# Optimization experiments

Measured on AMD Instinct MI355X. Metric: run time of the kernel, lower is better.

The kernel has to match this reference:

```python
import jax, jax.numpy as jnp
import numpy as np

N_NODES = 100000
N_EDGES = 1600000


def setup_inputs() -> dict:
    key = jax.random.key(0)
    ks = jax.random.split(key, 6)
    x = jax.random.normal(ks[0], (N_NODES, 128), dtype=jnp.float32)
    src = jax.random.randint(ks[1], (N_EDGES,), 0, N_NODES, dtype=jnp.int32)
    dst = jax.random.randint(ks[2], (N_EDGES,), 0, N_NODES, dtype=jnp.int32)
    # Glorot-ish scaled weights
    W1 = jax.random.normal(ks[3], (128, 64), dtype=jnp.float32) / np.sqrt(128.0)
    b1 = jnp.zeros((64,), dtype=jnp.float32)
    W2 = jax.random.normal(ks[4], (64, 64), dtype=jnp.float32) / np.sqrt(64.0)
    b2 = jnp.zeros((64,), dtype=jnp.float32)
    return {"x": x, "src": src, "dst": dst, "W1": W1, "b1": b1, "W2": W2, "b2": b2}


def _gcn_forward(x, src_f, dst_f, norm_src, norm_dst, W1, b1, W2, b2):
    n = x.shape[0]

    def conv(h, W, b):
        # weight-first (in_feats >= out_feats in DGL GraphConv): h W is cheap, aggregate small dim
        h = h @ W                                  # [N, d_out]
        h = h * norm_src[:, None]                  # D_out^{-1/2} on source side
        msg = h[src_f]                             # gather per edge [E+N, d_out]
        agg = jax.ops.segment_sum(msg, dst_f, num_segments=n)  # scatter-add to dst
        return agg * norm_dst[:, None] + b         # D_in^{-1/2} + bias

    h = jax.nn.relu(conv(x, W1, b1))
    return conv(h, W2, b2)


def reference(x, src, dst, W1, b1, W2, b2):
    n = x.shape[0]
    loop = jnp.arange(n, dtype=src.dtype)
    src_f = jnp.concatenate([src, loop])  # dgl.add_self_loop
    dst_f = jnp.concatenate([dst, loop])
    ones = jnp.ones(src_f.shape[0], dtype=x.dtype)
    out_deg = jax.ops.segment_sum(ones, src_f, num_segments=n)
    in_deg = jax.ops.segment_sum(ones, dst_f, num_segments=n)
    norm_src = jax.lax.rsqrt(out_deg)  # deg >= 1 due to self loops
    norm_dst = jax.lax.rsqrt(in_deg)
    return _gcn_forward(x, src_f, dst_f, norm_src, norm_dst, W1, b1, W2, b2)
```

## Files before the change

kernel.cpp:

```cpp
#include <hip/hip_runtime.h>
#include <hip/hip_fp16.h>

#define D 64
#define SLICE 25000
#define NBUCK 512
#define EPB 4096

typedef __attribute__((ext_vector_type(8))) short short8;
typedef __attribute__((ext_vector_type(4))) float floatx4;

__global__ __launch_bounds__(1024) void k_hist(const int* __restrict__ src,
                                               const int* __restrict__ dst,
                                               int* __restrict__ cnt_out,
                                               int* __restrict__ cnt_in,
                                               int E, int N) {
    __shared__ int h[SLICE];
    const int* idx = blockIdx.z ? dst : src;
    int* cnt       = blockIdx.z ? cnt_in : cnt_out;
    int lo = blockIdx.y * SLICE;
    int hi = min(lo + SLICE, N);
    int len = hi - lo;
    for (int i = threadIdx.x; i < len; i += 1024) h[i] = 0;
    __syncthreads();

    const int E4 = E >> 2;
    const int4* idx4 = (const int4*)idx;
    int stride = gridDim.x * 1024;
    for (int i = blockIdx.x * 1024 + threadIdx.x; i < E4; i += stride) {
        int4 v = idx4[i];
        if (v.x >= lo && v.x < hi) atomicAdd(&h[v.x - lo], 1);
        if (v.y >= lo && v.y < hi) atomicAdd(&h[v.y - lo], 1);
        if (v.z >= lo && v.z < hi) atomicAdd(&h[v.z - lo], 1);
        if (v.w >= lo && v.w < hi) atomicAdd(&h[v.w - lo], 1);
    }
    if (blockIdx.x == 0) {
        int e = E4 * 4 + threadIdx.x;
        if (e < E) {
            int v = idx[e];
            if (v >= lo && v < hi) atomicAdd(&h[v - lo], 1);
        }
    }
    __syncthreads();
    for (int i = threadIdx.x; i < len; i += 1024) {
        int c = h[i];
        if (c) atomicAdd(&cnt[lo + i], c);
    }
}

__global__ __launch_bounds__(256) void k_norm(const int* __restrict__ cnt,
                                              float* __restrict__ nrm, int n) {
    int i = blockIdx.x * 256 + threadIdx.x;
    if (i < n) nrm[i] = rsqrtf((float)cnt[i] + 1.0f);
}

__global__ __launch_bounds__(256) void k_scan1(const int* __restrict__ in,
                                               int* __restrict__ out,
                                               int* __restrict__ partials, int n) {
    __shared__ int s[256];
    int tid = threadIdx.x;
    int base = blockIdx.x * 1024 + tid * 4;
    int v[4];
#pragma unroll
    for (int j = 0; j < 4; ++j) v[j] = (base + j < n) ? in[base + j] : 0;
    int l1 = v[0] + v[1];
    int l2 = l1 + v[2];
    int total = l2 + v[3];
    s[tid] = total;
    __syncthreads();
    for (int off = 1; off < 256; off <<= 1) {
        int add = (tid >= off) ? s[tid - off] : 0;
        __syncthreads();
        s[tid] += add;
        __syncthreads();
    }
    int excl = s[tid] - total;
    if (base + 0 < n) out[base + 0] = excl;
    if (base + 1 < n) out[base + 1] = excl + v[0];
    if (base + 2 < n) out[base + 2] = excl + l1;
    if (base + 3 < n) out[base + 3] = excl + l2;
    if (tid == 255) partials[blockIdx.x] = s[255];
}

__global__ __launch_bounds__(256) void k_scan2(int* __restrict__ partials, int B,
                                               int* __restrict__ row_ptr, int N, int E) {
    __shared__ int s[256];
    int tid = threadIdx.x;
    int v = (tid < B) ? partials[tid] : 0;
    s[tid] = v;
    __syncthreads();
    for (int off = 1; off < 256; off <<= 1) {
        int add = (tid >= off) ? s[tid - off] : 0;
        __syncthreads();
        s[tid] += add;
        __syncthreads();
    }
    if (tid < B) partials[tid] = s[tid] - v;
    if (tid == 0) row_ptr[N] = E;
}

__global__ __launch_bounds__(256) void k_scan3(int* __restrict__ out,
                                               const int* __restrict__ partials, int n) {
    int off = partials[blockIdx.x];
    int base = blockIdx.x * 1024 + threadIdx.x * 4;
#pragma unroll
    for (int j = 0; j < 4; ++j)
        if (base + j < n) out[base + j] += off;
}

__global__ __launch_bounds__(256) void k_bin(const int* __restrict__ src,
                                             const int* __restrict__ dst,
                                             const int* __restrict__ row_ptr,
                                             int* __restrict__ bucket_cursor,
                                             unsigned long long* __restrict__ binned,
                                             int E) {
    __shared__ int cnt[NBUCK];
    __shared__ int bloc[NBUCK];
    __shared__ int lcur[NBUCK];
    __shared__ int gbase[NBUCK];
    __shared__ int ss[256];
    __shared__ unsigned long long stage[EPB];

    int tid = threadIdx.x;
    int start = blockIdx.x * EPB;
    int nloc = min(EPB, E - start);

    for (int i = tid; i < NBUCK; i += 256) cnt[i] = 0;
    __syncthreads();

#pragma unroll
    for (int r = 0; r < EPB / 256; ++r) {
        int idx = start + r * 256 + tid;
        if (idx < E) atomicAdd(&cnt[dst[idx] >> 8], 1);
    }
    __syncthreads();

    int a = cnt[2 * tid], b = cnt[2 * tid + 1];
    ss[tid] = a + b;
    __syncthreads();
    for (int off = 1; off < 256; off <<= 1) {
        int add = (tid >= off) ? ss[tid - off] : 0;
        __syncthreads();
        ss[tid] += add;
        __syncthreads();
    }
    int excl = ss[tid] - (a + b);
    bloc[2 * tid] = excl;           lcur[2 * tid] = excl;
    bloc[2 * tid + 1] = excl + a;   lcur[2 * tid + 1] = excl + a;
    __syncthreads();

    for (int bk = tid; bk < NBUCK; bk += 256) {
        int c = cnt[bk];
        gbase[bk] = c ? (atomicAdd(&bucket_cursor[bk], c) + row_ptr[bk << 8]) : 0;
    }
    __syncthreads();

#pragma unroll
    for (int r = 0; r < EPB / 256; ++r) {
        int idx = start + r * 256 + tid;
        if (idx < E) {
            int d = dst[idx];
            int p = atomicAdd(&lcur[d >> 8], 1);
            stage[p] = ((unsigned long long)(unsigned)d << 32) | (unsigned)src[idx];
        }
    }
    __syncthreads();

#pragma unroll
    for (int r = 0; r < EPB / 256; ++r) {
        int i = r * 256 + tid;
        if (i < nloc) {
            unsigned long long e = stage[i];
            int bk = (int)(e >> 40);
            binned[gbase[bk] + (i - bloc[bk])] = e;
        }
    }
}

__global__ __launch_bounds__(256) void k_bsort(const unsigned long long* __restrict__ binned,
                                               const int* __restrict__ row_ptr,
                                               int* __restrict__ csr, int N) {
    __shared__ int cur[256];
    int b = blockIdx.x;
    int n0 = b << 8;
    int tid = threadIdx.x;
    if (n0 + tid < N) cur[tid] = row_ptr[n0 + tid];
    __syncthreads();
    int base = row_ptr[n0];
    int c = row_ptr[min(n0 + 256, N)] - base;
    for (int k = tid; k < c; k += 256) {
        unsigned long long e = binned[base + k];
        int d = (int)(e >> 32);
        int s = (int)(e & 0xffffffffu);
        int p = atomicAdd(&cur[d - n0], 1);
        csr[p] = s;
    }
}

template <int K>
__global__ __launch_bounds__(256) void k_gemm_mfma(const float* __restrict__ hsrc,
                                                   const float* __restrict__ W,
                                                   const float* __restrict__ norm_src,
                                                   __half* __restrict__ t, int N) {
    constexpr int NKI = K / 32;
    __shared__ short Whi[NKI * 2048];
    __shared__ short Wlo[NKI * 2048];
    int tid = threadIdx.x;

    for (int f = tid; f < K * 64; f += 256) {
        int n  = f & 15;
        int j  = (f >> 4) & 7;
        int q  = (f >> 7) & 3;
        int ct = (f >> 9) & 3;
        int ki = f >> 11;
        int k = ki * 32 + q * 8 + j;
        int c = ct * 16 + n;
        float w = W[k * 64 + c];
        unsigned u = __float_as_uint(w);
        float l = w - __uint_as_float(u & 0xffff0000u);
        int idx = (((ki * 4 + ct) * 16 + n) * 4 + q) * 8 + j;
        Whi[idx] = (short)(u >> 16);
        Wlo[idx] = (short)(__float_as_uint(l) >> 16);
    }
    __syncthreads();

    int wave = tid >> 6, lane = tid & 63;
    int q = lane >> 4, n = lane & 15;
    int r0 = blockIdx.x * 64 + wave * 16;
    int rowc = min(r0 + n, N - 1);

    floatx4 acc[4] = {{0.f,0.f,0.f,0.f},{0.f,0.f,0.f,0.f},
                      {0.f,0.f,0.f,0.f},{0.f,0.f,0.f,0.f}};

    for (int ki = 0; ki < NKI; ++ki) {
        const float* ap = hsrc + (long long)rowc * K + ki * 32 + q * 8;
        float4 a0 = *(const float4*)ap;
        float4 a1 = *(const float4*)(ap + 4);
        float av[8] = {a0.x, a0.y, a0.z, a0.w, a1.x, a1.y, a1.z, a1.w};
        short8 ahi, alo;
#pragma unroll
        for (int j = 0; j < 8; ++j) {
            unsigned u = __float_as_uint(av[j]);
            float l = av[j] - __uint_as_float(u & 0xffff0000u);
            ahi[j] = (short)(u >> 16);
            alo[j] = (short)(__float_as_uint(l) >> 16);
        }
#pragma unroll
        for (int ct = 0; ct < 4; ++ct) {
            int bidx = (((ki * 4 + ct) * 16 + n) * 4 + q) * 8;
            short8 bhi = *(const short8*)&Whi[bidx];
            short8 blo = *(const short8*)&Wlo[bidx];
            acc[ct] = __builtin_amdgcn_mfma_f32_16x16x32_bf16(ahi, bhi, acc[ct], 0, 0, 0);
            acc[ct] = __builtin_amdgcn_mfma_f32_16x16x32_bf16(ahi, blo, acc[ct], 0, 0, 0);
            acc[ct] = __builtin_amdgcn_mfma_f32_16x16x32_bf16(alo, bhi, acc[ct], 0, 0, 0);
        }
    }

#pragma unroll
    for (int reg = 0; reg < 4; ++reg) {
        int orow = r0 + q * 4 + reg;
        if (orow < N) {
            float nrm = norm_src[orow];
#pragma unroll
            for (int ct = 0; ct < 4; ++ct)
                t[(long long)orow * 64 + ct * 16 + n] = __float2half(acc[ct][reg] * nrm);
        }
    }
}

__global__ __launch_bounds__(256) void k_agg(const int* __restrict__ row_ptr,
                                             const int* __restrict__ cnt,
                                             const int* __restrict__ csr,
                                             const __half* __restrict__ t,
                                             const float* __restrict__ norm_dst,
                                             const float* __restrict__ bias,
                                             float* __restrict__ out, int N, int do_relu) {
    int tid = threadIdx.x;
    int half_id = tid >> 5;
    int lane = tid & 31;
    int i = blockIdx.x * 8 + half_id;
    if (i >= N) return;
    const __half2* t2 = (const __half2*)t;
    int start = row_ptr[i], c = cnt[i];

    float2 sf = __half22float2(t2[i * 32 + lane]);
    float ax = sf.x, ay = sf.y;

    int j = 0;
    int pre = min(c, (4 - (start & 3)) & 3);
    for (; j < pre; ++j) {
        float2 f = __half22float2(t2[csr[start + j] * 32 + lane]);
        ax += f.x; ay += f.y;
    }
    for (; j + 8 <= c; j += 8) {
        int4 s4 = *(const int4*)&csr[start + j];
        int4 s5 = *(const int4*)&csr[start + j + 4];
        float2 f0 = __half22float2(t2[s4.x * 32 + lane]);
        float2 f1 = __half22float2(t2[s4.y * 32 + lane]);
        float2 f2 = __half22float2(t2[s4.z * 32 + lane]);
        float2 f3 = __half22float2(t2[s4.w * 32 + lane]);
        float2 f4 = __half22float2(t2[s5.x * 32 + lane]);
        float2 f5 = __half22float2(t2[s5.y * 32 + lane]);
        float2 f6 = __half22float2(t2[s5.z * 32 + lane]);
        float2 f7 = __half22float2(t2[s5.w * 32 + lane]);
        ax += ((f0.x + f1.x) + (f2.x + f3.x)) + ((f4.x + f5.x) + (f6.x + f7.x));
        ay += ((f0.y + f1.y) + (f2.y + f3.y)) + ((f4.y + f5.y) + (f6.y + f7.y));
    }
    for (; j + 4 <= c; j += 4) {
        int4 s4 = *(const int4*)&csr[start + j];
        float2 f0 = __half22float2(t2[s4.x * 32 + lane]);
        float2 f1 = __half22float2(t2[s4.y * 32 + lane]);
        float2 f2 = __half22float2(t2[s4.z * 32 + lane]);
        float2 f3 = __half22float2(t2[s4.w * 32 + lane]);
        ax += (f0.x + f1.x) + (f2.x + f3.x);
        ay += (f0.y + f1.y) + (f2.y + f3.y);
    }
    for (; j < c; ++j) {
        float2 f = __half22float2(t2[csr[start + j] * 32 + lane]);
        ax += f.x; ay += f.y;
    }

    float nrm = norm_dst[i];
    float2 bb = ((const float2*)bias)[lane];
    float vx = fmaf(ax, nrm, bb.x);
    float vy = fmaf(ay, nrm, bb.y);
    if (do_relu) { vx = fmaxf(vx, 0.f); vy = fmaxf(vy, 0.f); }
    float2 o; o.x = vx; o.y = vy;
    ((float2*)out)[i * 32 + lane] = o;
}

extern "C" void kernel_launch(void* const* d_in, const int* in_sizes, int n_in,
                              void* d_out, int out_size, void* d_ws, size_t ws_size,
                              hipStream_t stream) {
    const float* x   = (const float*)d_in[0];
    const int*   src = (const int*)d_in[1];
    const int*   dst = (const int*)d_in[2];
    const float* W1  = (const float*)d_in[3];
    const float* b1  = (const float*)d_in[4];
    const float* W2  = (const float*)d_in[5];
    const float* b2  = (const float*)d_in[6];
    float* out = (float*)d_out;

    const int N = in_sizes[0] / 128;
    const int E = in_sizes[1];

    int*   cnt_out  = (int*)d_ws;
    int*   cnt_in   = cnt_out + N;
    int*   row_ptr  = cnt_in + N;
    int*   partials = row_ptr + N + 1;
    float* norm_src = (float*)(partials + 1024);
    float* norm_dst = norm_src + N;
    long long toff = (5LL * N + 1025 + 63) & ~63LL;
    float* tbase    = (float*)d_ws + toff;
    float* h        = tbase + (long long)N * D;
    int*   csr      = (int*)(h + (long long)N * D);
    int*   bucket_cursor = csr + E;
    __half* t_h = (__half*)tbase;
    unsigned long long* binned = (unsigned long long*)tbase;

    const int B = (N + 1023) / 1024;
    const int NS = (N + SLICE - 1) / SLICE;
    const int NB = (N + 255) / 256;
    const int NBK = (E + EPB - 1) / EPB;

    hipMemsetAsync(cnt_out, 0, (size_t)2 * N * sizeof(int), stream);
    hipMemsetAsync(bucket_cursor, 0, (size_t)NBUCK * sizeof(int), stream);

    k_hist<<<dim3(8, NS, 2), 1024, 0, stream>>>(src, dst, cnt_out, cnt_in, E, N);
    k_norm<<<(2 * N + 255) / 256, 256, 0, stream>>>(cnt_out, norm_src, 2 * N);

    k_scan1<<<B, 256, 0, stream>>>(cnt_in, row_ptr, partials, N);
    k_scan2<<<1, 256, 0, stream>>>(partials, B, row_ptr, N, E);
    k_scan3<<<B, 256, 0, stream>>>(row_ptr, partials, N);

    k_bin<<<NBK, 256, 0, stream>>>(src, dst, row_ptr, bucket_cursor, binned, E);
    k_bsort<<<NB, 256, 0, stream>>>(binned, row_ptr, csr, N);

    k_gemm_mfma<128><<<(N + 63) / 64, 256, 0, stream>>>(x, W1, norm_src, t_h, N);
    k_agg<<<(N + 7) / 8, 256, 0, stream>>>(row_ptr, cnt_in, csr, t_h, norm_dst, b1, h, N, 1);

    k_gemm_mfma<64><<<(N + 63) / 64, 256, 0, stream>>>(h, W2, norm_src, t_h, N);
    k_agg<<<(N + 7) / 8, 256, 0, stream>>>(row_ptr, cnt_in, csr, t_h, norm_dst, b2, out, N, 0);
}
```

Measured before the change: 297.6 us.

## Split fp16 feature table into column slabs and parallelize aggregation over edges

```diff
diff --git a/kernel.cpp b/kernel.cpp
--- a/kernel.cpp
+++ b/kernel.cpp
@@ -262,7 +262,7 @@
             float nrm = norm_src[orow];
 #pragma unroll
             for (int ct = 0; ct < 4; ++ct)
-                t[(long long)orow * 64 + ct * 16 + n] = __float2half(acc[ct][reg] * nrm);
+                t[(ct * N + orow) * 16 + n] = __float2half(acc[ct][reg] * nrm);
         }
     }
 }
@@ -275,57 +275,59 @@
                                              const float* __restrict__ bias,
                                              float* __restrict__ out, int N, int do_relu) {
     int tid = threadIdx.x;
+    int g = blockIdx.x & 3;
+    int nb = blockIdx.x >> 2;
     int half_id = tid >> 5;
+    int i = nb * 8 + half_id;
+    if (i >= N) return;
     int lane = tid & 31;
-    int i = blockIdx.x * 8 + half_id;
-    if (i >= N) return;
-    const __half2* t2 = (const __half2*)t;
+    int e4 = lane >> 3;
+    int ch = lane & 7;
+
+    const __half2* t2 = (const __half2*)t + g * (N * 8);
     int start = row_ptr[i], c = cnt[i];
 
-    float2 sf = __half22float2(t2[i * 32 + lane]);
-    float ax = sf.x, ay = sf.y;
+    float2 sf = __half22float2(t2[i * 8 + ch]);
+    float ax = (e4 == 0) ? sf.x : 0.f;
+    float ay = (e4 == 0) ? sf.y : 0.f;
 
     int j = 0;
-    int pre = min(c, (4 - (start & 3)) & 3);
-    for (; j < pre; ++j) {
-        float2 f = __half22float2(t2[csr[start + j] * 32 + lane]);
-        ax += f.x; ay += f.y;
-    }
-    for (; j + 8 <= c; j += 8) {
-        int4 s4 = *(const int4*)&csr[start + j];
-        int4 s5 = *(const int4*)&csr[start + j + 4];
-        float2 f0 = __half22float2(t2[s4.x * 32 + lane]);
-        float2 f1 = __half22float2(t2[s4.y * 32 + lane]);
-        float2 f2 = __half22float2(t2[s4.z * 32 + lane]);
-        float2 f3 = __half22float2(t2[s4.w * 32 + lane]);
-        float2 f4 = __half22float2(t2[s5.x * 32 + lane]);
-        float2 f5 = __half22float2(t2[s5.y * 32 + lane]);
-        float2 f6 = __half22float2(t2[s5.z * 32 + lane]);
-        float2 f7 = __half22float2(t2[s5.w * 32 + lane]);
-        ax += ((f0.x + f1.x) + (f2.x + f3.x)) + ((f4.x + f5.x) + (f6.x + f7.x));
-        ay += ((f0.y + f1.y) + (f2.y + f3.y)) + ((f4.y + f5.y) + (f6.y + f7.y));
-    }
-    for (; j + 4 <= c; j += 4) {
-        int4 s4 = *(const int4*)&csr[start + j];
-        float2 f0 = __half22float2(t2[s4.x * 32 + lane]);
-        float2 f1 = __half22float2(t2[s4.y * 32 + lane]);
-        float2 f2 = __half22float2(t2[s4.z * 32 + lane]);
-        float2 f3 = __half22float2(t2[s4.w * 32 + lane]);
+    for (; j + 16 <= c; j += 16) {
+        int p = start + j + e4;
+        int s0 = csr[p];
+        int s1 = csr[p + 4];
+        int s2 = csr[p + 8];
+        int s3 = csr[p + 12];
+        float2 f0 = __half22float2(t2[s0 * 8 + ch]);
+        float2 f1 = __half22float2(t2[s1 * 8 + ch]);
+        float2 f2 = __half22float2(t2[s2 * 8 + ch]);
+        float2 f3 = __half22float2(t2[s3 * 8 + ch]);
         ax += (f0.x + f1.x) + (f2.x + f3.x);
         ay += (f0.y + f1.y) + (f2.y + f3.y);
     }
-    for (; j < c; ++j) {
-        float2 f = __half22float2(t2[csr[start + j] * 32 + lane]);
-        ax += f.x; ay += f.y;
-    }
-
-    float nrm = norm_dst[i];
-    float2 bb = ((const float2*)bias)[lane];
-    float vx = fmaf(ax, nrm, bb.x);
-    float vy = fmaf(ay, nrm, bb.y);
-    if (do_relu) { vx = fmaxf(vx, 0.f); vy = fmaxf(vy, 0.f); }
-    float2 o; o.x = vx; o.y = vy;
-    ((float2*)out)[i * 32 + lane] = o;
+    for (; j + 4 <= c; j += 4) {
+        int s0 = csr[start + j + e4];
+        float2 f0 = __half22float2(t2[s0 * 8 + ch]);
+        ax += f0.x; ay += f0.y;
+    }
+    if (e4 < c - j) {
+        int s0 = csr[start + j + e4];
+        float2 f0 = __half22float2(t2[s0 * 8 + ch]);
+        ax += f0.x; ay += f0.y;
+    }
+
+    ax += __shfl_xor(ax, 8);  ay += __shfl_xor(ay, 8);
+    ax += __shfl_xor(ax, 16); ay += __shfl_xor(ay, 16);
+
+    if (e4 == 0) {
+        float nrm = norm_dst[i];
+        float2 bb = ((const float2*)bias)[g * 8 + ch];
+        float vx = fmaf(ax, nrm, bb.x);
+        float vy = fmaf(ay, nrm, bb.y);
+        if (do_relu) { vx = fmaxf(vx, 0.f); vy = fmaxf(vy, 0.f); }
+        float2 o; o.x = vx; o.y = vy;
+        ((float2*)out)[i * 32 + g * 8 + ch] = o;
+    }
 }
 
 extern "C" void kernel_launch(void* const* d_in, const int* in_sizes, int n_in,
@@ -375,9 +377,11 @@
     k_bin<<<NBK, 256, 0, stream>>>(src, dst, row_ptr, bucket_cursor, binned, E);
     k_bsort<<<NB, 256, 0, stream>>>(binned, row_ptr, csr, N);
 
+    const int AGG_BLOCKS = ((N + 7) / 8) * 4;
+
     k_gemm_mfma<128><<<(N + 63) / 64, 256, 0, stream>>>(x, W1, norm_src, t_h, N);
-    k_agg<<<(N + 7) / 8, 256, 0, stream>>>(row_ptr, cnt_in, csr, t_h, norm_dst, b1, h, N, 1);
+    k_agg<<<AGG_BLOCKS, 256, 0, stream>>>(row_ptr, cnt_in, csr, t_h, norm_dst, b1, h, N, 1);
 
     k_gemm_mfma<64><<<(N + 63) / 64, 256, 0, stream>>>(h, W2, norm_src, t_h, N);
-    k_agg<<<(N + 7) / 8, 256, 0, stream>>>(row_ptr, cnt_in, csr, t_h, norm_dst, b2, out, N, 0);
-}
+    k_agg<<<AGG_BLOCKS, 256, 0, stream>>>(row_ptr, cnt_in, csr, t_h, norm_dst, b2, out, N, 0);
+}
```

New measurement: 393.9 us. 32.4% more time.
